# Kernel tuning notes

Measured on AMD Instinct MI355X. Metric: run time of the kernel, lower is better.

The kernel has to match this reference:

```python
import jax, jax.numpy as jnp
import numpy as np

N, IN_DIM, HID, OUT, E = 20000, 1024, 512, 128, 160000


def _xavier(key, fan_out, fan_in):
    a = (6.0 / (fan_in + fan_out)) ** 0.5
    return jax.random.uniform(key, (fan_out, fan_in), jnp.float32, -a, a)


def setup_inputs() -> dict:
    key = jax.random.key(0)
    ks = jax.random.split(key, 8)
    features = jax.random.normal(ks[0], (N, IN_DIM), jnp.float32)
    edge_index = jax.random.randint(ks[1], (2, E), 0, N, jnp.int64)
    W1 = _xavier(ks[2], HID, IN_DIM)   # conv1.lin.weight [out,in]
    b1 = jnp.zeros((HID,), jnp.float32)
    W2 = _xavier(ks[3], OUT, HID)      # conv2.lin.weight
    b2 = jnp.zeros((OUT,), jnp.float32)
    b3 = jnp.zeros((HID,), jnp.float32)  # conv3 bias (weight tied = W2.T)
    b4 = jnp.zeros((IN_DIM,), jnp.float32)  # conv4 bias (weight tied = W1.T)
    head1 = _xavier(ks[4], OUT, OUT)
    return dict(features=features, edge_index=edge_index, W1=W1, b1=b1,
                W2=W2, b2=b2, b3=b3, b4=b4, head1=head1)


def _gcn_conv(x, W, b, src, dst, norm, n):
    # GCNConv: transform then symmetric-normalized neighbor aggregation
    h = x @ W.T                       # [N, out]
    msg = h[src] * norm[:, None]      # [E', out] gathered + scaled
    out = jax.ops.segment_sum(msg, dst, num_segments=n)
    return out + b


def reference(features, edge_index, W1, b1, W2, b2, b3, b4, head1):
    n = features.shape[0]
    loops = jnp.arange(n, dtype=edge_index.dtype)
    src = jnp.concatenate([edge_index[0], loops])  # add self-loops
    dst = jnp.concatenate([edge_index[1], loops])
    deg = jax.ops.segment_sum(jnp.ones_like(dst, dtype=features.dtype), dst,
                              num_segments=n)
    dinv = jnp.where(deg > 0, deg ** -0.5, 0.0)
    norm = dinv[src] * dinv[dst]

    h1 = _gcn_conv(features, W1, b1, src, dst, norm, n)
    h2 = _gcn_conv(h1, W2, b2, src, dst, norm, n)
    z = h2 @ head1
    # tied weights: conv3.W = W2^T, conv4.W = W1^T
    h3 = _gcn_conv(z, W2.T, b3, src, dst, norm, n)
    h4 = _gcn_conv(h3, W1.T, b4, src, dst, norm, n)
    return z, h2, h4
```

## Files before the change

### kernel.cpp

```cpp
#include <hip/hip_runtime.h>

typedef short   short8  __attribute__((ext_vector_type(8)));
typedef unsigned short ushort8 __attribute__((ext_vector_type(8)));
typedef float   floatx4 __attribute__((ext_vector_type(4)));

__device__ __forceinline__ float bf2f(unsigned short h) {
    unsigned int u = ((unsigned int)h) << 16;
    return __builtin_bit_cast(float, u);
}
__device__ __forceinline__ unsigned short f2bf(float f) {
    unsigned int u = __builtin_bit_cast(unsigned int, f);
    u += 0x7fffu + ((u >> 16) & 1u);
    return (unsigned short)(u >> 16);
}


__global__ __launch_bounds__(256) void k_detect_f32(const unsigned short* __restrict__ X,
                                                    int nPairs, int* __restrict__ flags) {
    int i = blockIdx.x * 256 + threadIdx.x;
    if (i < nPairs) {
        unsigned short w = X[2 * i];
        if ((w & 0x7F80u) == 0x7F80u) atomicOr(&flags[0], 1);
    }
}

__global__ __launch_bounds__(256) void k_detect_i32(const int* __restrict__ ei,
                                                    int E, int* __restrict__ flags) {
    int i = blockIdx.x * 256 + threadIdx.x;
    if (i < E) {
        if (ei[2 * i + 1] != 0) atomicOr(&flags[1], 1);
    }
}


__global__ __launch_bounds__(256) void k_cvt_f32(const void* __restrict__ in,
                                                 float* __restrict__ out, int n,
                                                 const int* __restrict__ flags) {
    int i = blockIdx.x * 256 + threadIdx.x;
    if (i < n)
        out[i] = flags[0] ? ((const float*)in)[i] : bf2f(((const unsigned short*)in)[i]);
}

__global__ __launch_bounds__(256) void k_tcvt(const void* __restrict__ in,
                                              unsigned short* __restrict__ out,
                                              int R, int C, const int* __restrict__ flags) {
    int idx = blockIdx.x * 256 + threadIdx.x;
    if (idx >= R * C) return;
    int r = idx / C, c = idx - r * C;
    unsigned short v = flags[0] ? f2bf(((const float*)in)[idx])
                                : ((const unsigned short*)in)[idx];
    out[(long)c * R + r] = v;
}


__global__ __launch_bounds__(256) void k_count(const int* __restrict__ ei, int E, int n,
                                               const int* __restrict__ flags,
                                               int* __restrict__ deg) {
    int e = blockIdx.x * 256 + threadIdx.x;
    if (e >= E) return;
    int sh = (flags[1] == 0) ? 1 : 0;
    int d = ei[(long)(E + e) << sh];
    if ((unsigned)d < (unsigned)n) atomicAdd(&deg[d], 1);
}

__global__ __launch_bounds__(256) void k_dinv(const int* __restrict__ deg,
                                              float* __restrict__ dinv, int n) {
    int i = blockIdx.x * 256 + threadIdx.x;
    if (i < n) dinv[i] = rsqrtf((float)(deg[i] + 1));
}

__global__ __launch_bounds__(1024) void k_scan(const int* __restrict__ deg,
                                               int* __restrict__ row_start,
                                               int* __restrict__ cursor, int n) {
    __shared__ int sums[1024];
    int t = threadIdx.x;
    int CH = (n + 1 + 1023) / 1024;
    int base = t * CH;
    int s = 0;
    for (int i = 0; i < CH; i++) {
        int idx = base + i;
        if (idx < n) s += deg[idx];
    }
    sums[t] = s;
    __syncthreads();
    for (int off = 1; off < 1024; off <<= 1) {
        int v = (t >= off) ? sums[t - off] : 0;
        __syncthreads();
        if (t >= off) sums[t] += v;
        __syncthreads();
    }
    int run = (t > 0) ? sums[t - 1] : 0;
    for (int i = 0; i < CH; i++) {
        int idx = base + i;
        if (idx < n) {
            row_start[idx] = run;
            cursor[idx] = run;
            run += deg[idx];
        } else if (idx == n) {
            row_start[n] = run;
        }
    }
}

__global__ __launch_bounds__(256) void k_fill(const int* __restrict__ ei, int E, int n,
                                              const int* __restrict__ flags,
                                              int* __restrict__ cursor,
                                              int* __restrict__ csr) {
    int e = blockIdx.x * 256 + threadIdx.x;
    if (e >= E) return;
    int sh = (flags[1] == 0) ? 1 : 0;
    int s = ei[(long)e << sh];
    int d = ei[(long)(E + e) << sh];
    if ((unsigned)d >= (unsigned)n || (unsigned)s >= (unsigned)n) return;
    int p = atomicAdd(&cursor[d], 1);
    csr[p] = s;
}


__device__ __forceinline__ ushort8 ld8(const void* p, long e, bool f32) {
    if (!f32) return *(const ushort8*)((const unsigned short*)p + e);
    const float* f = (const float*)p + e;
    ushort8 r;
#pragma unroll
    for (int i = 0; i < 8; i++) r[i] = f2bf(f[i]);
    return r;
}

__global__ __launch_bounds__(256) void gemm_nt(const void* __restrict__ A, int aMaybeF32,
                                               const void* __restrict__ Bt, int bMaybeF32,
                                               void* __restrict__ Cv, long coff,
                                               const float* __restrict__ bias,
                                               int M, int N, int K, int finalOut,
                                               const int* __restrict__ flags) {
    constexpr int BM = 128, BN = 64, BK = 32, LDT = 40;
    __shared__ unsigned short sA[BM * LDT];
    __shared__ unsigned short sB[BN * LDT];
    const bool af32 = aMaybeF32 && flags[0];
    const bool bf32 = bMaybeF32 && flags[0];
    const bool of32 = finalOut && flags[0];
    const bool hasb = bias != nullptr;
    const int t = threadIdx.x;
    const int m0 = blockIdx.y * BM;
    const int n0 = blockIdx.x * BN;
    const int w = t >> 6;
    const int lane = t & 63;
    const int id = lane & 15;
    const int q = lane >> 4;

    floatx4 acc[2][4];
    for (int s = 0; s < 2; s++)
        for (int j = 0; j < 4; j++) acc[s][j] = (floatx4)0.0f;

    const int ar = t >> 2;
    const int ac = (t & 3) * 8;

    for (int k0 = 0; k0 < K; k0 += BK) {
        long r0 = min(m0 + ar, M - 1);
        long r1 = min(m0 + ar + 64, M - 1);
        ushort8 va0 = ld8(A, r0 * K + k0 + ac, af32);
        ushort8 va1 = ld8(A, r1 * K + k0 + ac, af32);
        ushort8 vb  = ld8(Bt, (long)(n0 + ar) * K + k0 + ac, bf32);
        __syncthreads();
        *(ushort8*)(sA + ar * LDT + ac) = va0;
        *(ushort8*)(sA + (ar + 64) * LDT + ac) = va1;
        *(ushort8*)(sB + ar * LDT + ac) = vb;
        __syncthreads();

        short8 afrag[2], bfrag[4];
        for (int s = 0; s < 2; s++)
            afrag[s] = *(const short8*)(sA + (32 * w + 16 * s + id) * LDT + q * 8);
        for (int j = 0; j < 4; j++)
            bfrag[j] = *(const short8*)(sB + (16 * j + id) * LDT + q * 8);
        for (int s = 0; s < 2; s++)
            for (int j = 0; j < 4; j++)
                acc[s][j] = __builtin_amdgcn_mfma_f32_16x16x32_bf16(
                    afrag[s], bfrag[j], acc[s][j], 0, 0, 0);
    }

    for (int s = 0; s < 2; s++)
        for (int j = 0; j < 4; j++) {
            int col = n0 + 16 * j + id;
            float bv = hasb ? bias[col] : 0.0f;
            for (int r = 0; r < 4; r++) {
                int row = m0 + 32 * w + 16 * s + q * 4 + r;
                if (row < M) {
                    float v = acc[s][j][r] + bv;
                    if (of32) ((float*)Cv)[coff + (long)row * N + col] = v;
                    else ((unsigned short*)Cv)[coff + (long)row * N + col] = f2bf(v);
                }
            }
        }
}


template <int D>
__global__ __launch_bounds__(256) void k_agg(const unsigned short* __restrict__ T,
                                             const int* __restrict__ rs,
                                             const int* __restrict__ csr,
                                             const float* __restrict__ dinv,
                                             const float* __restrict__ bias,
                                             unsigned short* __restrict__ O, int n) {
    constexpr int TPN = D / 8;
    constexpr int NPB = 256 / TPN;
    int lt = threadIdx.x % TPN;
    int node = blockIdx.x * NPB + threadIdx.x / TPN;
    if (node >= n) return;
    int off = lt * 8;
    float acc[8];
#pragma unroll
    for (int i = 0; i < 8; i++) acc[i] = 0.0f;
    int beg = rs[node], end = rs[node + 1];
    for (int j = beg; j < end; j++) {
        int s = csr[j];
        if ((unsigned)s >= (unsigned)n) continue;
        float wgt = dinv[s];
        ushort8 v = *(const ushort8*)(T + (long)s * D + off);
#pragma unroll
        for (int i = 0; i < 8; i++) acc[i] += wgt * bf2f(v[i]);
    }
    float di = dinv[node];
    ushort8 sv = *(const ushort8*)(T + (long)node * D + off);
    ushort8 o;
#pragma unroll
    for (int i = 0; i < 8; i++) {
        float r = di * (acc[i] + di * bf2f(sv[i])) + (bias ? bias[off + i] : 0.0f);
        o[i] = f2bf(r);
    }
    *(ushort8*)(O + (long)node * D + off) = o;
}


__global__ __launch_bounds__(256) void k_out(const unsigned short* __restrict__ z,
                                             const unsigned short* __restrict__ h2,
                                             void* __restrict__ out, int nOut,
                                             const int* __restrict__ flags) {
    int i = blockIdx.x * 256 + threadIdx.x;
    if (i >= 2 * nOut) return;
    unsigned short v = (i < nOut) ? z[i] : h2[i - nOut];
    if (flags[0]) ((float*)out)[i] = bf2f(v);
    else ((unsigned short*)out)[i] = v;
}


extern "C" void kernel_launch(void* const* d_in, const int* in_sizes, int n_in,
                              void* d_out, int out_size, void* d_ws, size_t ws_size,
                              hipStream_t stream) {
    const int IN  = in_sizes[7];
    const int HID = in_sizes[3];
    const int OUT = in_sizes[5];
    const int Nn  = in_sizes[0] / IN;
    const int E   = in_sizes[1] / 2;

    const void* X   = d_in[0];
    const int*  ei  = (const int*)d_in[1];
    const void* W1  = d_in[2];
    const void* b1  = d_in[3];
    const void* W2  = d_in[4];
    const void* b2  = d_in[5];
    const void* b3  = d_in[6];
    const void* b4  = d_in[7];
    const void* Hd1 = d_in[8];

    char* base = (char*)d_ws;
    size_t o = 0;
    auto carve = [&](size_t bytes) -> char* {
        char* p = base + o;
        o = (o + bytes + 255) & ~(size_t)255;
        return p;
    };
    int*   flags  = (int*)carve(2 * 4);
    int*   deg    = (int*)carve((size_t)Nn * 4);
    int*   rowst  = (int*)carve((size_t)(Nn + 1) * 4);
    int*   cursor = (int*)carve((size_t)Nn * 4);
    float* dinv   = (float*)carve((size_t)Nn * 4);
    int*   csr    = (int*)carve((size_t)E * 4);
    float* biasf  = (float*)carve((size_t)(HID + OUT + HID + IN) * 4);
    float* bc1 = biasf, *bc2 = biasf + HID, *bc3 = biasf + HID + OUT,
         *bc4 = biasf + HID + OUT + HID;
    unsigned short* W1t  = (unsigned short*)carve((size_t)IN * HID * 2);
    unsigned short* W2t  = (unsigned short*)carve((size_t)HID * OUT * 2);
    unsigned short* H1t  = (unsigned short*)carve((size_t)OUT * OUT * 2);
    unsigned short* t1   = (unsigned short*)carve((size_t)Nn * HID * 2);
    unsigned short* h1   = (unsigned short*)carve((size_t)Nn * HID * 2);
    unsigned short* h3   = (unsigned short*)carve((size_t)Nn * HID * 2);
    unsigned short* t2   = (unsigned short*)carve((size_t)Nn * OUT * 2);
    unsigned short* h2ws = (unsigned short*)carve((size_t)Nn * OUT * 2);
    unsigned short* zws  = (unsigned short*)carve((size_t)Nn * OUT * 2);

    hipMemsetAsync(flags, 0, 8, stream);
    hipMemsetAsync(deg, 0, (size_t)Nn * 4, stream);
    int nPairs = 1 << 20;
    k_detect_f32<<<(nPairs + 255) / 256, 256, 0, stream>>>((const unsigned short*)X, nPairs, flags);
    k_detect_i32<<<(E + 255) / 256, 256, 0, stream>>>(ei, E, flags);

    k_cvt_f32<<<(HID + 255) / 256, 256, 0, stream>>>(b1, bc1, HID, flags);
    k_cvt_f32<<<(OUT + 255) / 256, 256, 0, stream>>>(b2, bc2, OUT, flags);
    k_cvt_f32<<<(HID + 255) / 256, 256, 0, stream>>>(b3, bc3, HID, flags);
    k_cvt_f32<<<(IN + 255) / 256, 256, 0, stream>>>(b4, bc4, IN, flags);

    k_tcvt<<<(HID * IN + 255) / 256, 256, 0, stream>>>(W1, W1t, HID, IN, flags);
    k_tcvt<<<(OUT * HID + 255) / 256, 256, 0, stream>>>(W2, W2t, OUT, HID, flags);
    k_tcvt<<<(OUT * OUT + 255) / 256, 256, 0, stream>>>(Hd1, H1t, OUT, OUT, flags);

    k_count<<<(E + 255) / 256, 256, 0, stream>>>(ei, E, Nn, flags, deg);
    k_dinv<<<(Nn + 255) / 256, 256, 0, stream>>>(deg, dinv, Nn);
    k_scan<<<1, 1024, 0, stream>>>(deg, rowst, cursor, Nn);
    k_fill<<<(E + 255) / 256, 256, 0, stream>>>(ei, E, Nn, flags, cursor, csr);

    dim3 blk(256);
    auto ggrid = [&](int Ncols) { return dim3((Ncols + 63) / 64, (Nn + 127) / 128); };
    const long zOff = 0, h2Off = (long)Nn * OUT, h4Off = (long)Nn * OUT * 2;

    gemm_nt<<<ggrid(HID), blk, 0, stream>>>(X, 1, W1, 1, t1, 0, nullptr, Nn, HID, IN, 0, flags);
    k_agg<512><<<(Nn * 64 + 255) / 256, blk, 0, stream>>>(t1, rowst, csr, dinv, bc1, h1, Nn);

    gemm_nt<<<ggrid(OUT), blk, 0, stream>>>(h1, 0, W2, 1, t2, 0, nullptr, Nn, OUT, HID, 0, flags);
    k_agg<128><<<(Nn * 16 + 255) / 256, blk, 0, stream>>>(t2, rowst, csr, dinv, bc2, h2ws, Nn);

    gemm_nt<<<ggrid(OUT), blk, 0, stream>>>(h2ws, 0, H1t, 0, zws, 0, nullptr, Nn, OUT, OUT, 0, flags);

    k_agg<128><<<(Nn * 16 + 255) / 256, blk, 0, stream>>>(zws, rowst, csr, dinv, nullptr, t2, Nn);
    gemm_nt<<<ggrid(HID), blk, 0, stream>>>(t2, 0, W2t, 0, h3, 0, bc3, Nn, HID, OUT, 0, flags);

    k_agg<512><<<(Nn * 64 + 255) / 256, blk, 0, stream>>>(h3, rowst, csr, dinv, nullptr, t1, Nn);
    gemm_nt<<<ggrid(IN), blk, 0, stream>>>(t1, 0, W1t, 0, d_out, h4Off, bc4, Nn, IN, HID, 1, flags);

    k_out<<<(2 * (int)h2Off + 255) / 256, blk, 0, stream>>>(zws, h2ws, d_out, (int)h2Off, flags);
}
```

Measured before the change: 605.6 us.

## Enlarge GEMM tiles to 128x128x64 with fragment-ordered LDS and grouped block swizzle

The GEMM tile grows from 128x64x32 to 128x128x64, so each wave computes a 64x64 quadrant with 16 MFMA accumulators. Shared memory is now laid out in MFMA fragment order, so loads and stores are contiguous per lane and no padding is needed. Blocks are launched on a 1-D grid and remapped so groups of 8 M-tiles share an N-column, which should improve L2 reuse. The intent is to raise arithmetic intensity and cut global and LDS traffic per FLOP, at the cost of more registers and lower occupancy.

```diff
diff --git a/kernel.cpp b/kernel.cpp
--- a/kernel.cpp
+++ b/kernel.cpp
@@ -130,61 +130,83 @@
                                                const void* __restrict__ Bt, int bMaybeF32,
                                                void* __restrict__ Cv, long coff,
                                                const float* __restrict__ bias,
-                                               int M, int N, int K, int finalOut,
+                                               int M, int N, int K, int nc, int finalOut,
                                                const int* __restrict__ flags) {
-    constexpr int BM = 128, BN = 64, BK = 32, LDT = 40;
-    __shared__ unsigned short sA[BM * LDT];
-    __shared__ unsigned short sB[BN * LDT];
+    constexpr int BM = 128, BN = 128, BK = 64;
+    __shared__ unsigned short sA[BM * BK];
+    __shared__ unsigned short sB[BN * BK];
+    const int nm = (M + BM - 1) / BM;
+    int l = blockIdx.x;
+    int g = l / (8 * nc);
+    int r = l % (8 * nc);
+    int mi = g * 8 + (r & 7);
+    if (mi >= nm) return;
+    int ci = r >> 3;
+    const int m0 = mi * BM, n0 = ci * BN;
     const bool af32 = aMaybeF32 && flags[0];
     const bool bf32 = bMaybeF32 && flags[0];
     const bool of32 = finalOut && flags[0];
-    const bool hasb = bias != nullptr;
     const int t = threadIdx.x;
-    const int m0 = blockIdx.y * BM;
-    const int n0 = blockIdx.x * BN;
-    const int w = t >> 6;
-    const int lane = t & 63;
-    const int id = lane & 15;
-    const int q = lane >> 4;
-
-    floatx4 acc[2][4];
-    for (int s = 0; s < 2; s++)
-        for (int j = 0; j < 4; j++) acc[s][j] = (floatx4)0.0f;
-
-    const int ar = t >> 2;
-    const int ac = (t & 3) * 8;
+    const int w = t >> 6, lane = t & 63, id = lane & 15, q = lane >> 4;
+    const int mq = w >> 1, nq = w & 1;
+
+    floatx4 acc[4][4];
+    for (int i = 0; i < 4; i++)
+        for (int j = 0; j < 4; j++) acc[i][j] = (floatx4)0.0f;
+
+    long aoff[4], boff[4];
+    int loff[4];
+#pragma unroll
+    for (int c = 0; c < 4; c++) {
+        int u = w * 4 + c;
+        int T = u >> 1, kk = u & 1;
+        long arow = m0 + 16 * T + id; if (arow > M - 1) arow = M - 1;
+        long brow = n0 + 16 * T + id; if (brow > N - 1) brow = N - 1;
+        aoff[c] = arow * K + kk * 32 + q * 8;
+        boff[c] = brow * K + kk * 32 + q * 8;
+        loff[c] = u * 512 + lane * 8;
+    }
 
     for (int k0 = 0; k0 < K; k0 += BK) {
-        long r0 = min(m0 + ar, M - 1);
-        long r1 = min(m0 + ar + 64, M - 1);
-        ushort8 va0 = ld8(A, r0 * K + k0 + ac, af32);
-        ushort8 va1 = ld8(A, r1 * K + k0 + ac, af32);
-        ushort8 vb  = ld8(Bt, (long)(n0 + ar) * K + k0 + ac, bf32);
+        ushort8 va[4], vb[4];
+#pragma unroll
+        for (int c = 0; c < 4; c++) {
+            va[c] = ld8(A, aoff[c] + k0, af32);
+            vb[c] = ld8(Bt, boff[c] + k0, bf32);
+        }
         __syncthreads();
-        *(ushort8*)(sA + ar * LDT + ac) = va0;
-        *(ushort8*)(sA + (ar + 64) * LDT + ac) = va1;
-        *(ushort8*)(sB + ar * LDT + ac) = vb;
+#pragma unroll
+        for (int c = 0; c < 4; c++) {
+            *(ushort8*)(sA + loff[c]) = va[c];
+            *(ushort8*)(sB + loff[c]) = vb[c];
+        }
         __syncthreads();
-
-        short8 afrag[2], bfrag[4];
-        for (int s = 0; s < 2; s++)
-            afrag[s] = *(const short8*)(sA + (32 * w + 16 * s + id) * LDT + q * 8);
-        for (int j = 0; j < 4; j++)
-            bfrag[j] = *(const short8*)(sB + (16 * j + id) * LDT + q * 8);
-        for (int s = 0; s < 2; s++)
+#pragma unroll
+        for (int kk = 0; kk < 2; kk++) {
+            short8 af[4], bf[4];
+#pragma unroll
+            for (int i = 0; i < 4; i++)
+                af[i] = *(const short8*)(sA + ((4 * mq + i) * 2 + kk) * 512 + lane * 8);
+#pragma unroll
             for (int j = 0; j < 4; j++)
-                acc[s][j] = __builtin_amdgcn_mfma_f32_16x16x32_bf16(
-                    afrag[s], bfrag[j], acc[s][j], 0, 0, 0);
-    }
-
-    for (int s = 0; s < 2; s++)
+                bf[j] = *(const short8*)(sB + ((4 * nq + j) * 2 + kk) * 512 + lane * 8);
+#pragma unroll
+            for (int i = 0; i < 4; i++)
+#pragma unroll
+                for (int j = 0; j < 4; j++)
+                    acc[i][j] = __builtin_amdgcn_mfma_f32_16x16x32_bf16(
+                        af[i], bf[j], acc[i][j], 0, 0, 0);
+        }
+    }
+
+    for (int i = 0; i < 4; i++)
         for (int j = 0; j < 4; j++) {
-            int col = n0 + 16 * j + id;
-            float bv = hasb ? bias[col] : 0.0f;
-            for (int r = 0; r < 4; r++) {
-                int row = m0 + 32 * w + 16 * s + q * 4 + r;
+            int col = n0 + 64 * nq + 16 * j + id;
+            float bv = bias ? bias[col] : 0.0f;
+            for (int rr = 0; rr < 4; rr++) {
+                int row = m0 + 64 * mq + 16 * i + 4 * q + rr;
                 if (row < M) {
-                    float v = acc[s][j][r] + bv;
+                    float v = acc[i][j][rr] + bv;
                     if (of32) ((float*)Cv)[coff + (long)row * N + col] = v;
                     else ((unsigned short*)Cv)[coff + (long)row * N + col] = f2bf(v);
                 }
@@ -308,22 +330,28 @@
     k_fill<<<(E + 255) / 256, 256, 0, stream>>>(ei, E, Nn, flags, cursor, csr);
 
     dim3 blk(256);
-    auto ggrid = [&](int Ncols) { return dim3((Ncols + 63) / 64, (Nn + 127) / 128); };
-    const long zOff = 0, h2Off = (long)Nn * OUT, h4Off = (long)Nn * OUT * 2;
-
-    gemm_nt<<<ggrid(HID), blk, 0, stream>>>(X, 1, W1, 1, t1, 0, nullptr, Nn, HID, IN, 0, flags);
+    const int nm = (Nn + 127) / 128;
+    const int G  = (nm + 7) / 8;
+    auto ggrid = [&](int N_) { int nc = N_ / 128; return dim3(G * 8 * nc); };
+
+    gemm_nt<<<ggrid(HID), blk, 0, stream>>>(X, 1, W1, 1, t1, 0, nullptr,
+                                            Nn, HID, IN, HID / 128, 0, flags);
     k_agg<512><<<(Nn * 64 + 255) / 256, blk, 0, stream>>>(t1, rowst, csr, dinv, bc1, h1, Nn);
 
-    gemm_nt<<<ggrid(OUT), blk, 0, stream>>>(h1, 0, W2, 1, t2, 0, nullptr, Nn, OUT, HID, 0, flags);
+    gemm_nt<<<ggrid(OUT), blk, 0, stream>>>(h1, 0, W2, 1, t2, 0, nullptr,
+                                            Nn, OUT, HID, OUT / 128, 0, flags);
     k_agg<128><<<(Nn * 16 + 255) / 256, blk, 0, stream>>>(t2, rowst, csr, dinv, bc2, h2ws, Nn);
 
-    gemm_nt<<<ggrid(OUT), blk, 0, stream>>>(h2ws, 0, H1t, 0, zws, 0, nullptr, Nn, OUT, OUT, 0, flags);
+    gemm_nt<<<ggrid(OUT), blk, 0, stream>>>(h2ws, 0, H1t, 0, zws, 0, nullptr,
+                                            Nn, OUT, OUT, OUT / 128, 0, flags);
 
     k_agg<128><<<(Nn * 16 + 255) / 256, blk, 0, stream>>>(zws, rowst, csr, dinv, nullptr, t2, Nn);
-    gemm_nt<<<ggrid(HID), blk, 0, stream>>>(t2, 0, W2t, 0, h3, 0, bc3, Nn, HID, OUT, 0, flags);
+    gemm_nt<<<ggrid(HID), blk, 0, stream>>>(t2, 0, W2t, 0, h3, 0, bc3,
+                                            Nn, HID, OUT, HID / 128, 0, flags);
 
     k_agg<512><<<(Nn * 64 + 255) / 256, blk, 0, stream>>>(h3, rowst, csr, dinv, nullptr, t1, Nn);
-    gemm_nt<<<ggrid(IN), blk, 0, stream>>>(t1, 0, W1t, 0, d_out, h4Off, bc4, Nn, IN, HID, 1, flags);
-
-    k_out<<<(2 * (int)h2Off + 255) / 256, blk, 0, stream>>>(zws, h2ws, d_out, (int)h2Off, flags);
-}
+    gemm_nt<<<ggrid(IN), blk, 0, stream>>>(t1, 0, W1t, 0, d_out, (long)Nn * OUT * 2, bc4,
+                                           Nn, IN, HID, IN / 128, 1, flags);
+
+    k_out<<<(2 * Nn * OUT + 255) / 256, blk, 0, stream>>>(zws, h2ws, d_out, Nn * OUT, flags);
+}
```

Measured after the change: 995.4 us. 64.4% more time.
